# Performance work log

Hardware: AMD Instinct MI355X
Metric: run time of the kernel (lower is better)

Reference implementation:

```python
import jax, jax.numpy as jnp
import numpy as np

B, S, E, H, V2, L, T = 512, 49, 1024, 1024, 16, 64, 48
D_IN = E + V2 + 1 + L  # LSTM input size = 1105


def setup_inputs() -> dict:
    key = jax.random.key(0)
    ks = jax.random.split(key, 16)
    sd_h = 1.0 / np.sqrt(H)
    u = lambda k, shape, s: jax.random.uniform(k, shape, jnp.float32, -s, s)
    length = jax.random.randint(ks[0], (B,), 1, T + 1).at[0].set(T)
    return {
        'image': jax.random.normal(ks[1], (B, S, E), jnp.float32),
        'view_position': jax.random.uniform(ks[2], (B, V2), jnp.float32),
        'label': jax.random.uniform(ks[3], (B, T + 1, L), jnp.float32),
        'length': length,
        'fc_h_w': u(ks[4], (H, E), 1.0 / np.sqrt(E)),
        'fc_h_b': u(ks[5], (H,), 1.0 / np.sqrt(E)),
        'fc_m_w': u(ks[6], (H, E), 1.0 / np.sqrt(E)),
        'fc_m_b': u(ks[7], (H,), 1.0 / np.sqrt(E)),
        'w_ih': u(ks[8], (4 * H, D_IN), sd_h),
        'w_hh': u(ks[9], (4 * H, H), sd_h),
        'b_ih': u(ks[10], (4 * H,), sd_h),
        'b_hh': u(ks[11], (4 * H,), sd_h),
        'fc_w': u(ks[12], (L + H + 2, H), sd_h),
        'fc_b': u(ks[13], (L + H + 2,), sd_h),
    }


def reference(image, view_position, label, length,
              fc_h_w, fc_h_b, fc_m_w, fc_m_b,
              w_ih, w_hh, b_ih, b_hh, fc_w, fc_b):
    image_mean = image.mean(1)                              # (B, E)
    h0 = jnp.tanh(image_mean @ fc_h_w.T + fc_h_b)           # (B, H)
    m0 = jnp.tanh(image_mean @ fc_m_w.T + fc_m_b)

    # teacher-forced label input: zeros at t=0, then label[:, t-1]
    lab_in = jnp.concatenate([jnp.zeros((B, 1, L), jnp.float32),
                              label[:, :T - 1]], 1)          # (B, T, L)
    lab_in = jnp.transpose(lab_in, (1, 0, 2))                # (T, B, L)
    t_idx = jnp.arange(T)
    begin = (t_idx == 0).astype(jnp.float32)[:, None, None] * jnp.ones((T, B, 1), jnp.float32)
    mask = (t_idx[:, None] < length[None, :]).astype(jnp.float32)[:, :, None]  # (T, B, 1)

    def step(carry, xs):
        h, m = carry
        lab_t, begin_t, mask_t = xs
        x = jnp.concatenate([image_mean, view_position, begin_t, lab_t], 1)  # (B, D_IN)
        gates = x @ w_ih.T + b_ih + h @ w_hh.T + b_hh                        # (B, 4H)
        i, f, g, o = jnp.split(gates, 4, axis=1)
        m_new = jax.nn.sigmoid(f) * m + jax.nn.sigmoid(i) * jnp.tanh(g)
        h_new = jax.nn.sigmoid(o) * jnp.tanh(m_new)
        out = h_new @ fc_w.T + fc_b                                          # (B, L+H+2)
        _lab = jax.nn.sigmoid(out[:, :L]) * mask_t
        _topic = jax.nn.relu(out[:, L:L + H]) * mask_t
        _stop = jax.nn.sigmoid(out[:, L + H:L + H + 1]) * mask_t
        _temp = jnp.exp(out[:, L + H + 1:]) * mask_t
        return (h_new, m_new), (_lab, _topic, _stop, _temp)

    _, (lab_o, topic_o, stop_o, temp_o) = jax.lax.scan(step, (h0, m0), (lab_in, begin, mask))
    # shapes: (T, B, L), (T, B, H), (T, B, 1), (T, B, 1) -- matches pad_sequence layout
    return lab_o, topic_o, stop_o, temp_o
```

## Files before the change

kernel.cpp:

```cpp
#include <hip/hip_runtime.h>
#include <hip/hip_bf16.h>
#include <cstdint>


typedef __bf16 bf16_t;
typedef bf16_t bf16x8 __attribute__((ext_vector_type(8)));
typedef bf16_t bf16x4 __attribute__((ext_vector_type(4)));
typedef float  f32x4  __attribute__((ext_vector_type(4)));

#define Bn    512
#define Sn    49
#define En    1024
#define Hn    1024
#define Ln    64
#define Tn    48
#define DINn  1105
#define NOn   1090
#define HLD   1088
#define HSTEP 557056

#define BM   64
#define LDSP 72

__device__ __forceinline__ float sigm(float x){ return 1.0f / (1.0f + __expf(-x)); }

__global__ __launch_bounds__(256) void k_mean(const float* __restrict__ image,
                                              bf16_t* __restrict__ imb){
  int b  = blockIdx.x;
  int e0 = threadIdx.x * 4;
  const float* p = image + (size_t)b * (Sn * En) + e0;
  float4 acc = make_float4(0.f, 0.f, 0.f, 0.f);
  for (int s = 0; s < Sn; ++s){
    float4 v = *reinterpret_cast<const float4*>(p + (size_t)s * En);
    acc.x += v.x; acc.y += v.y; acc.z += v.z; acc.w += v.w;
  }
  const float inv = 1.0f / 49.0f;
  bf16x4 o;
  o[0] = (bf16_t)(acc.x * inv); o[1] = (bf16_t)(acc.y * inv);
  o[2] = (bf16_t)(acc.z * inv); o[3] = (bf16_t)(acc.w * inv);
  *reinterpret_cast<bf16x4*>(imb + (size_t)b * En + e0) = o;
}

__global__ __launch_bounds__(256) void k_convert(
    const float* __restrict__ w_hh,  const float* __restrict__ fc_h_w,
    const float* __restrict__ fc_m_w,const float* __restrict__ fc_w,
    const float* __restrict__ label, const float* __restrict__ w_ih,
    bf16_t* __restrict__ whht,  bf16_t* __restrict__ fchwb,
    bf16_t* __restrict__ fcmwb, bf16_t* __restrict__ fcwb,
    bf16_t* __restrict__ wimgb, bf16_t* __restrict__ hs){
  const int E0 = 32 * 17 * 16 * 512;
  const int E1 = E0 + 1024 * 1024;
  const int E2 = E1 + 1024 * 1024;
  const int E3 = E2 + 1090 * 1024;
  const int E4 = E3 + 4096 * 1024;
  const int E5 = E4 + 48 * 512 * 64;
  int stride = gridDim.x * blockDim.x;
  for (int i = blockIdx.x * blockDim.x + threadIdx.x; i < E5; i += stride){
    if (i < E0){
      int e = i & 7, l = (i >> 3) & 63, g = (i >> 9) & 15;
      int rest = i >> 13;
      int kt = rest % 17, cbb = rest / 17;
      int wv = g >> 2, ni = (g >> 1) & 1, kk = g & 1;
      int n = wv * 1024 + cbb * 32 + ni * 16 + (l & 15);
      int k = kt * 64 + kk * 32 + (l >> 4) * 8 + e;
      float v = (k < 1024) ? w_hh[(size_t)n * 1024 + k]
                           : w_ih[(size_t)n * DINn + 1041 + (k - 1024)];
      whht[i] = (bf16_t)v;
    } else if (i < E1){ int j = i - E0; fchwb[j] = (bf16_t)fc_h_w[j]; }
    else if (i < E2){ int j = i - E1; fcmwb[j] = (bf16_t)fc_m_w[j]; }
    else if (i < E3){ int j = i - E2; fcwb[j]  = (bf16_t)fc_w[j]; }
    else if (i < E4){
      int j = i - E3; int n = j >> 10, k = j & 1023;
      wimgb[j] = (bf16_t)w_ih[(size_t)n * DINn + k];
    } else {
      int j = i - E4;
      int t = j >> 15, rem = j & 32767, row = rem >> 6, c = rem & 63;
      float v = (t == 0) ? 0.f : label[(size_t)row * (Sn * Ln) + (t - 1) * 64 + c];
      hs[((size_t)t * 512 + row) * HLD + 1024 + c] = (bf16_t)v;
    }
  }
}

__global__ __launch_bounds__(256) void k_vpc(const float* __restrict__ w_ih,
                                             const float* __restrict__ vp,
                                             const float* __restrict__ b_ih,
                                             const float* __restrict__ b_hh,
                                             float* __restrict__ xconst){
  int idx = blockIdx.x * 256 + threadIdx.x;
  int b = idx >> 12, n = idx & 4095;
  float acc = b_ih[n] + b_hh[n];
  const float* w = w_ih + (size_t)n * DINn + En;
  const float* v = vp + b * 16;
  #pragma unroll
  for (int j = 0; j < 16; ++j) acc += v[j] * w[j];
  xconst[idx] = acc;
}

__device__ __forceinline__ void stageAp(bf16_t* sA, const bf16_t* gptr, int ld, int tid){
  #pragma unroll
  for (int i = 0; i < 2; ++i){
    int idx = tid + i * 256;
    int r = idx >> 3, v = idx & 7;
    *reinterpret_cast<bf16x8*>(sA + r * LDSP + v * 8) =
      *reinterpret_cast<const bf16x8*>(gptr + (size_t)r * ld + v * 8);
  }
}

__device__ __forceinline__ void mma_tile(const bf16_t* sA, const bf16_t* sB,
                                         f32x4 (&acc)[4][2], int lane, int w){
  int lr = lane & 15;
  int lk = (lane >> 4) * 8;
  #pragma unroll
  for (int kk = 0; kk < 2; ++kk){
    bf16x8 a[4], bb[2];
    #pragma unroll
    for (int mi = 0; mi < 4; ++mi)
      a[mi] = *reinterpret_cast<const bf16x8*>(sA + (mi * 16 + lr) * LDSP + kk * 32 + lk);
    #pragma unroll
    for (int ni = 0; ni < 2; ++ni)
      bb[ni] = *reinterpret_cast<const bf16x8*>(sB + (w * 32 + ni * 16 + lr) * LDSP + kk * 32 + lk);
    #pragma unroll
    for (int mi = 0; mi < 4; ++mi)
      #pragma unroll
      for (int ni = 0; ni < 2; ++ni)
        acc[mi][ni] = __builtin_amdgcn_mfma_f32_16x16x32_bf16(a[mi], bb[ni], acc[mi][ni], 0, 0, 0);
  }
}

__global__ __launch_bounds__(256) void k_init_gemm(
    const bf16_t* __restrict__ imb,  const bf16_t* __restrict__ fchw,
    const bf16_t* __restrict__ fcmw, const bf16_t* __restrict__ wimg,
    const float* __restrict__ fc_h_b,const float* __restrict__ fc_m_b,
    bf16_t* __restrict__ h0, float* __restrict__ m0, float* __restrict__ xconst){
  __shared__ __align__(16) unsigned char smem[(BM + 128) * LDSP * 2];
  bf16_t* sA = (bf16_t*)smem;
  bf16_t* sB = (bf16_t*)(smem + BM * LDSP * 2);
  int tid = threadIdx.x;
  int cb = blockIdx.x, rb = blockIdx.y;
  int nBase = cb * 128;
  const bf16_t* Bsrc; int nOff;
  if      (nBase < 1024){ Bsrc = fchw; nOff = nBase; }
  else if (nBase < 2048){ Bsrc = fcmw; nOff = nBase - 1024; }
  else                  { Bsrc = wimg; nOff = nBase - 2048; }

  f32x4 acc[4][2] = {};
  int lane = tid & 63, w = tid >> 6;
  for (int kt = 0; kt < 16; ++kt){
    stageAp(sA, imb + (size_t)(rb * 64) * 1024 + kt * 64, 1024, tid);
    #pragma unroll
    for (int i = 0; i < 4; ++i){
      int idx = tid + i * 256;
      int r = idx >> 3, v = idx & 7;
      *reinterpret_cast<bf16x8*>(sB + r * LDSP + v * 8) =
        *reinterpret_cast<const bf16x8*>(Bsrc + (size_t)(nOff + r) * 1024 + kt * 64 + v * 8);
    }
    __syncthreads();
    mma_tile(sA, sB, acc, lane, w);
    __syncthreads();
  }
  int lr = lane & 15, lg = lane >> 4;
  #pragma unroll
  for (int mi = 0; mi < 4; ++mi)
    #pragma unroll
    for (int ni = 0; ni < 2; ++ni)
      #pragma unroll
      for (int r = 0; r < 4; ++r){
        int ng   = nBase + w * 32 + ni * 16 + lr;
        int rowg = rb * 64 + mi * 16 + lg * 4 + r;
        float v = acc[mi][ni][r];
        if (ng < 1024){
          h0[(size_t)rowg * HLD + ng] = (bf16_t)tanhf(v + fc_h_b[ng]);
        } else if (ng < 2048){
          int n = ng - 1024;
          m0[(size_t)rowg * 1024 + n] = tanhf(v + fc_m_b[n]);
        } else {
          int n = ng - 2048;
          xconst[(size_t)rowg * 4096 + n] += v;
        }
      }
}

__global__ __launch_bounds__(256) void k_step(
    const bf16_t* __restrict__ hin,
    bf16_t* __restrict__ hout,
    const bf16_t* __restrict__ whht,
    const float* __restrict__ xconst,
    const float* __restrict__ w_ih,
    float* __restrict__ m,
    int t){
  __shared__ __align__(16) unsigned char smem[33792];
  float* gbuf = (float*)smem;
  int tid = threadIdx.x;
  int cb = blockIdx.x, rb = blockIdx.y;
  int lane = tid & 63, w = tid >> 6;
  int rsub = lane >> 3;
  int usw  = (((lane & 7) ^ rsub) & 7) * 8;
  int lr = lane & 15;
  int key = lr & 7;
  int ub = lane >> 4;
  f32x4 acc[4][2] = {};

  const bf16_t* bbase = whht + (((size_t)cb * 17) << 13) + ((w * 4) << 9) + lane * 8;
  bf16x8 breg[4][2][2];

  auto stageA = [&](int slot, int kt){
    char* base = (char*)smem + slot * 8192;
    #pragma unroll
    for (int c = 0; c < 2; ++c){
      int q = w * 2 + c;
      int r = q * 8 + rsub;
      const bf16_t* g = hin + (size_t)(rb * 64 + r) * HLD + kt * 64 + usw;
      __builtin_amdgcn_global_load_lds((const void*)g, (void*)(base + q * 1024), 16, 0, 0);
    }
  };
  auto loadB = [&](int slot, int kt){
    #pragma unroll
    for (int ni = 0; ni < 2; ++ni)
      #pragma unroll
      for (int kk = 0; kk < 2; ++kk)
        breg[slot][ni][kk] = *reinterpret_cast<const bf16x8*>(
            bbase + ((size_t)kt << 13) + ((ni * 2 + kk) << 9));
  };
  auto compute = [&](int kt){
    const bf16_t* sA = (const bf16_t*)((const char*)smem + (kt & 3) * 8192);
    const int s = kt & 3;
    #pragma unroll
    for (int kk = 0; kk < 2; ++kk){
      int uo = ((kk * 4 + ub) ^ key) * 8;
      bf16x8 a[4];
      #pragma unroll
      for (int mi = 0; mi < 4; ++mi)
        a[mi] = *reinterpret_cast<const bf16x8*>(sA + (mi * 16 + lr) * 64 + uo);
      #pragma unroll
      for (int mi = 0; mi < 4; ++mi){
        acc[mi][0] = __builtin_amdgcn_mfma_f32_16x16x32_bf16(a[mi], breg[s][0][kk], acc[mi][0], 0, 0, 0);
        acc[mi][1] = __builtin_amdgcn_mfma_f32_16x16x32_bf16(a[mi], breg[s][1][kk], acc[mi][1], 0, 0, 0);
      }
    }
  };

  loadB(0, 0); stageA(0, 0);
  loadB(1, 1); stageA(1, 1);
  loadB(2, 2); stageA(2, 2);

  #pragma unroll
  for (int kt = 0; kt < 14; ++kt){
    loadB((kt + 3) & 3, kt + 3);
    stageA((kt + 3) & 3, kt + 3);
    asm volatile("s_waitcnt vmcnt(18)" ::: "memory");
    __builtin_amdgcn_sched_barrier(0);
    __builtin_amdgcn_s_barrier();
    compute(kt);
    __builtin_amdgcn_s_barrier();
  }
  asm volatile("s_waitcnt vmcnt(12)" ::: "memory");
  __builtin_amdgcn_sched_barrier(0);
  __builtin_amdgcn_s_barrier();
  compute(14);
  __builtin_amdgcn_s_barrier();
  asm volatile("s_waitcnt vmcnt(6)" ::: "memory");
  __builtin_amdgcn_sched_barrier(0);
  __builtin_amdgcn_s_barrier();
  compute(15);
  __builtin_amdgcn_s_barrier();
  asm volatile("s_waitcnt vmcnt(0)" ::: "memory");
  __builtin_amdgcn_sched_barrier(0);
  __builtin_amdgcn_s_barrier();
  compute(16);
  __syncthreads();

  int lg = lane >> 4;
  #pragma unroll
  for (int mi = 0; mi < 4; ++mi)
    #pragma unroll
    for (int ni = 0; ni < 2; ++ni)
      #pragma unroll
      for (int r = 0; r < 4; ++r){
        int cl = ni * 16 + lr;
        int ng = w * 1024 + cb * 32 + cl;
        int rl = mi * 16 + lg * 4 + r;
        int rowg = rb * 64 + rl;
        float v = acc[mi][ni][r] + xconst[(size_t)rowg * 4096 + ng];
        if (t == 0) v += w_ih[(size_t)ng * DINn + 1040];
        gbuf[(w * 64 + rl) * 33 + cl] = v;
      }
  __syncthreads();
  #pragma unroll
  for (int rep = 0; rep < 8; ++rep){
    int cell = tid + rep * 256;
    int rl = cell >> 5, cl = cell & 31;
    float gi = gbuf[(0 * 64 + rl) * 33 + cl];
    float gf = gbuf[(1 * 64 + rl) * 33 + cl];
    float gg = gbuf[(2 * 64 + rl) * 33 + cl];
    float go = gbuf[(3 * 64 + rl) * 33 + cl];
    int rowg = rb * 64 + rl, colg = cb * 32 + cl;
    size_t o = (size_t)rowg * 1024 + colg;
    float mo = m[o];
    float mn = sigm(gf) * mo + sigm(gi) * tanhf(gg);
    m[o] = mn;
    float hn = sigm(go) * tanhf(mn);
    hout[(size_t)rowg * HLD + colg] = (bf16_t)hn;
  }
}

__global__ __launch_bounds__(256) void k_out(
    const bf16_t* __restrict__ h,
    const bf16_t* __restrict__ fcwb,
    const float* __restrict__ fc_b, const int* __restrict__ length,
    float* __restrict__ out){
  __shared__ __align__(16) unsigned char smem[73728];
  int tid = threadIdx.x;
  int id  = blockIdx.x;
  int xcd = id & 7;
  int rem = id >> 3;
  int cb  = rem % 9;
  int grp = rem / 9;
  int rb  = xcd + 8 * grp;
  int lane = tid & 63, w = tid >> 6;
  int rsub = lane >> 3;
  int usw  = (((lane & 7) ^ rsub) & 7) * 8;
  int lr = lane & 15;
  int key = lr & 7;
  int ub = lane >> 4;
  f32x4 acc[4][2] = {};

  auto stage = [&](int buf, int kt){
    char* base = (char*)smem + buf * 24576;
    #pragma unroll
    for (int c = 0; c < 2; ++c){
      int q = w * 2 + c;
      int r = q * 8 + rsub;
      const bf16_t* g = h + (size_t)(rb * 64 + r) * HLD + kt * 64 + usw;
      __builtin_amdgcn_global_load_lds((const void*)g, (void*)(base + q * 1024), 16, 0, 0);
    }
    #pragma unroll
    for (int c = 0; c < 4; ++c){
      int q = w * 4 + c;
      int r = q * 8 + rsub;
      int n = cb * 128 + r;
      int ncl = (n < NOn) ? n : (NOn - 1);
      const bf16_t* g = fcwb + (size_t)ncl * 1024 + kt * 64 + usw;
      __builtin_amdgcn_global_load_lds((const void*)g, (void*)(base + 8192 + q * 1024), 16, 0, 0);
    }
  };
  auto compute = [&](int buf){
    const bf16_t* sA = (const bf16_t*)((const char*)smem + buf * 24576);
    const bf16_t* sB = sA + 4096;
    #pragma unroll
    for (int kk = 0; kk < 2; ++kk){
      int uo = ((kk * 4 + ub) ^ key) * 8;
      bf16x8 a[4], bb[2];
      #pragma unroll
      for (int mi = 0; mi < 4; ++mi)
        a[mi] = *reinterpret_cast<const bf16x8*>(sA + (mi * 16 + lr) * 64 + uo);
      #pragma unroll
      for (int ni = 0; ni < 2; ++ni)
        bb[ni] = *reinterpret_cast<const bf16x8*>(sB + (w * 32 + ni * 16 + lr) * 64 + uo);
      #pragma unroll
      for (int mi = 0; mi < 4; ++mi)
        #pragma unroll
        for (int ni = 0; ni < 2; ++ni)
          acc[mi][ni] = __builtin_amdgcn_mfma_f32_16x16x32_bf16(a[mi], bb[ni], acc[mi][ni], 0, 0, 0);
    }
  };

  stage(0, 0);
  stage(1, 1);
  #pragma unroll
  for (int kt = 0; kt < 14; ++kt){
    stage((kt + 2) % 3, kt + 2);
    asm volatile("s_waitcnt vmcnt(12)" ::: "memory");
    __builtin_amdgcn_sched_barrier(0);
    __builtin_amdgcn_s_barrier();
    compute(kt % 3);
    __builtin_amdgcn_s_barrier();
  }
  asm volatile("s_waitcnt vmcnt(6)" ::: "memory");
  __builtin_amdgcn_sched_barrier(0);
  __builtin_amdgcn_s_barrier();
  compute(14 % 3);
  __builtin_amdgcn_s_barrier();
  asm volatile("s_waitcnt vmcnt(0)" ::: "memory");
  __builtin_amdgcn_sched_barrier(0);
  __builtin_amdgcn_s_barrier();
  compute(15 % 3);

  int lg = lane >> 4;
  #pragma unroll
  for (int mi = 0; mi < 4; ++mi)
    #pragma unroll
    for (int ni = 0; ni < 2; ++ni)
      #pragma unroll
      for (int r = 0; r < 4; ++r){
        int ng = cb * 128 + w * 32 + ni * 16 + lr;
        if (ng >= NOn) continue;
        int rg = rb * 64 + mi * 16 + lg * 4 + r;
        int tt = rg >> 9, b = rg & 511;
        float v = acc[mi][ni][r] + fc_b[ng];
        float mask = (tt < length[b]) ? 1.0f : 0.0f;
        if      (ng < 64)    out[(size_t)rg * 64 + ng] = sigm(v) * mask;
        else if (ng < 1088)  out[(size_t)1572864 + (size_t)rg * 1024 + (ng - 64)] = fmaxf(v, 0.f) * mask;
        else if (ng == 1088) out[(size_t)26738688 + rg] = sigm(v) * mask;
        else                 out[(size_t)26763264 + rg] = __expf(v) * mask;
      }
}

extern "C" void kernel_launch(void* const* d_in, const int* in_sizes, int n_in,
                              void* d_out, int out_size, void* d_ws, size_t ws_size,
                              hipStream_t stream){
  const float* image  = (const float*)d_in[0];
  const float* vp     = (const float*)d_in[1];
  const float* label  = (const float*)d_in[2];
  const int*   length = (const int*)  d_in[3];
  const float* fc_h_w = (const float*)d_in[4];
  const float* fc_h_b = (const float*)d_in[5];
  const float* fc_m_w = (const float*)d_in[6];
  const float* fc_m_b = (const float*)d_in[7];
  const float* w_ih   = (const float*)d_in[8];
  const float* w_hh   = (const float*)d_in[9];
  const float* b_ih   = (const float*)d_in[10];
  const float* b_hh   = (const float*)d_in[11];
  const float* fc_w   = (const float*)d_in[12];
  const float* fc_b   = (const float*)d_in[13];
  float* out = (float*)d_out;

  char* ws = (char*)d_ws;
  bf16_t* imb    = (bf16_t*)(ws + 0);
  bf16_t* hs     = (bf16_t*)(ws + 1048576);
  float*  m      = (float*) (ws + 55640064);
  float*  xconst = (float*) (ws + 57737216);
  bf16_t* whht   = (bf16_t*)(ws + 66125824);
  bf16_t* wimgb  = (bf16_t*)(ws + 75038720);
  bf16_t* fchwb  = (bf16_t*)(ws + 83427328);
  bf16_t* fcmwb  = (bf16_t*)(ws + 85524480);
  bf16_t* fcwb   = (bf16_t*)(ws + 87621632);

  k_mean   <<<dim3(512),  dim3(256), 0, stream>>>(image, imb);
  k_convert<<<dim3(2048), dim3(256), 0, stream>>>(w_hh, fc_h_w, fc_m_w, fc_w, label, w_ih,
                                                  whht, fchwb, fcmwb, fcwb, wimgb, hs);
  k_vpc    <<<dim3(8192), dim3(256), 0, stream>>>(w_ih, vp, b_ih, b_hh, xconst);
  k_init_gemm<<<dim3(48, 8), dim3(256), 0, stream>>>(imb, fchwb, fcmwb, wimgb,
                                                     fc_h_b, fc_m_b, hs, m, xconst);
  for (int t = 0; t < Tn; ++t){
    k_step<<<dim3(32, 8), dim3(256), 0, stream>>>(hs + (size_t)t * HSTEP,
                                                  hs + (size_t)(t + 1) * HSTEP,
                                                  whht, xconst, w_ih, m, t);
  }
  k_out<<<dim3(3456), dim3(256), 0, stream>>>(hs + (size_t)HSTEP, fcwb, fc_b, length, out);
}
```

Measured before the change: 923.0 us.

## Stage entire A tile into LDS up front instead of 4-slot pipeline

Replaces the 4-deep software pipeline in the LSTM step GEMM with a single bulk load of all 17 K-tiles of the hidden state into LDS, followed by one wait and barrier. B fragments are then loaded per tile inside the compute loop. The aim is to drop the per-iteration barriers and waitcnt synchronisation. In exchange, LDS use grows to about 136 KB per block, which limits occupancy to one block per CU. B loads are also no longer prefetched ahead of use, so their latency is exposed.

```diff
diff --git a/kernel.cpp b/kernel.cpp
--- a/kernel.cpp
+++ b/kernel.cpp
@@ -188,7 +188,7 @@
     const float* __restrict__ w_ih,
     float* __restrict__ m,
     int t){
-  __shared__ __align__(16) unsigned char smem[33792];
+  __shared__ __align__(16) unsigned char smem[139264];
   float* gbuf = (float*)smem;
   int tid = threadIdx.x;
   int cb = blockIdx.x, rb = blockIdx.y;
@@ -201,10 +201,10 @@
   f32x4 acc[4][2] = {};
 
   const bf16_t* bbase = whht + (((size_t)cb * 17) << 13) + ((w * 4) << 9) + lane * 8;
-  bf16x8 breg[4][2][2];
-
-  auto stageA = [&](int slot, int kt){
-    char* base = (char*)smem + slot * 8192;
+
+  #pragma unroll
+  for (int kt = 0; kt < 17; ++kt){
+    char* base = (char*)smem + kt * 8192;
     #pragma unroll
     for (int c = 0; c < 2; ++c){
       int q = w * 2 + c;
@@ -212,18 +212,18 @@
       const bf16_t* g = hin + (size_t)(rb * 64 + r) * HLD + kt * 64 + usw;
       __builtin_amdgcn_global_load_lds((const void*)g, (void*)(base + q * 1024), 16, 0, 0);
     }
-  };
-  auto loadB = [&](int slot, int kt){
-    #pragma unroll
-    for (int ni = 0; ni < 2; ++ni)
-      #pragma unroll
-      for (int kk = 0; kk < 2; ++kk)
-        breg[slot][ni][kk] = *reinterpret_cast<const bf16x8*>(
-            bbase + ((size_t)kt << 13) + ((ni * 2 + kk) << 9));
-  };
-  auto compute = [&](int kt){
-    const bf16_t* sA = (const bf16_t*)((const char*)smem + (kt & 3) * 8192);
-    const int s = kt & 3;
+  }
+  asm volatile("s_waitcnt vmcnt(0)" ::: "memory");
+  __builtin_amdgcn_sched_barrier(0);
+  __builtin_amdgcn_s_barrier();
+
+  #pragma unroll
+  for (int kt = 0; kt < 17; ++kt){
+    bf16x8 b00 = *reinterpret_cast<const bf16x8*>(bbase + ((size_t)kt << 13) + (0 << 9));
+    bf16x8 b01 = *reinterpret_cast<const bf16x8*>(bbase + ((size_t)kt << 13) + (1 << 9));
+    bf16x8 b10 = *reinterpret_cast<const bf16x8*>(bbase + ((size_t)kt << 13) + (2 << 9));
+    bf16x8 b11 = *reinterpret_cast<const bf16x8*>(bbase + ((size_t)kt << 13) + (3 << 9));
+    const bf16_t* sA = (const bf16_t*)((const char*)smem + kt * 8192);
     #pragma unroll
     for (int kk = 0; kk < 2; ++kk){
       int uo = ((kk * 4 + ub) ^ key) * 8;
@@ -231,42 +231,15 @@
       #pragma unroll
       for (int mi = 0; mi < 4; ++mi)
         a[mi] = *reinterpret_cast<const bf16x8*>(sA + (mi * 16 + lr) * 64 + uo);
+      bf16x8 bk0 = (kk == 0) ? b00 : b01;
+      bf16x8 bk1 = (kk == 0) ? b10 : b11;
       #pragma unroll
       for (int mi = 0; mi < 4; ++mi){
-        acc[mi][0] = __builtin_amdgcn_mfma_f32_16x16x32_bf16(a[mi], breg[s][0][kk], acc[mi][0], 0, 0, 0);
-        acc[mi][1] = __builtin_amdgcn_mfma_f32_16x16x32_bf16(a[mi], breg[s][1][kk], acc[mi][1], 0, 0, 0);
+        acc[mi][0] = __builtin_amdgcn_mfma_f32_16x16x32_bf16(a[mi], bk0, acc[mi][0], 0, 0, 0);
+        acc[mi][1] = __builtin_amdgcn_mfma_f32_16x16x32_bf16(a[mi], bk1, acc[mi][1], 0, 0, 0);
       }
     }
-  };
-
-  loadB(0, 0); stageA(0, 0);
-  loadB(1, 1); stageA(1, 1);
-  loadB(2, 2); stageA(2, 2);
-
-  #pragma unroll
-  for (int kt = 0; kt < 14; ++kt){
-    loadB((kt + 3) & 3, kt + 3);
-    stageA((kt + 3) & 3, kt + 3);
-    asm volatile("s_waitcnt vmcnt(18)" ::: "memory");
-    __builtin_amdgcn_sched_barrier(0);
-    __builtin_amdgcn_s_barrier();
-    compute(kt);
-    __builtin_amdgcn_s_barrier();
-  }
-  asm volatile("s_waitcnt vmcnt(12)" ::: "memory");
-  __builtin_amdgcn_sched_barrier(0);
-  __builtin_amdgcn_s_barrier();
-  compute(14);
-  __builtin_amdgcn_s_barrier();
-  asm volatile("s_waitcnt vmcnt(6)" ::: "memory");
-  __builtin_amdgcn_sched_barrier(0);
-  __builtin_amdgcn_s_barrier();
-  compute(15);
-  __builtin_amdgcn_s_barrier();
-  asm volatile("s_waitcnt vmcnt(0)" ::: "memory");
-  __builtin_amdgcn_sched_barrier(0);
-  __builtin_amdgcn_s_barrier();
-  compute(16);
+  }
   __syncthreads();
 
   int lg = lane >> 4;
```

Measured after the change: 910.6 us. No clear change (-1.3%).
